# Optimization experiments

Hardware: AMD Instinct MI355X
Metric: run time of the kernel (lower is better)

## Reference

```python
import jax, jax.numpy as jnp
import numpy as np

H = 64  # hidden_dim


def _gru_cell(x, h, W_ih, W_hh, b_ih, b_hh):
    # PyTorch GRU gate order: reset (r), update (z), new (n)
    gx = x @ W_ih.T + b_ih            # [B, 3H]
    gh = h @ W_hh.T + b_hh            # [B, 3H]
    xr, xz, xn = jnp.split(gx, 3, axis=-1)
    hr, hz, hn = jnp.split(gh, 3, axis=-1)
    r = jax.nn.sigmoid(xr + hr)
    z = jax.nn.sigmoid(xz + hz)
    n = jnp.tanh(xn + r * hn)
    return (1.0 - z) * n + z * h


def setup_inputs() -> dict:
    key = jax.random.key(0)
    ks = jax.random.split(key, 11)
    B, T, F_in, A = 1024, 512, 128, 18
    s = 0.05
    return {
        "state": jax.random.normal(ks[0], (B, T, F_in), dtype=jnp.float32),
        "W_ih_l0": jax.random.normal(ks[1], (3 * H, F_in), dtype=jnp.float32) * s,
        "W_hh_l0": jax.random.normal(ks[2], (3 * H, H), dtype=jnp.float32) * s,
        "b_ih_l0": jax.random.normal(ks[3], (3 * H,), dtype=jnp.float32) * s,
        "b_hh_l0": jax.random.normal(ks[4], (3 * H,), dtype=jnp.float32) * s,
        "W_ih_l1": jax.random.normal(ks[5], (3 * H, H), dtype=jnp.float32) * s,
        "W_hh_l1": jax.random.normal(ks[6], (3 * H, H), dtype=jnp.float32) * s,
        "b_ih_l1": jax.random.normal(ks[7], (3 * H,), dtype=jnp.float32) * s,
        "b_hh_l1": jax.random.normal(ks[8], (3 * H,), dtype=jnp.float32) * s,
        "fc3_w": jax.random.normal(ks[9], (A, H), dtype=jnp.float32) * s,
        "fc3_b": jax.random.normal(ks[10], (A,), dtype=jnp.float32) * s,
    }


def reference(state, W_ih_l0, W_hh_l0, b_ih_l0, b_hh_l0,
              W_ih_l1, W_hh_l1, b_ih_l1, b_hh_l1, fc3_w, fc3_b):
    B = state.shape[0]
    h0 = jnp.zeros((B, H), dtype=state.dtype)
    h1 = jnp.zeros((B, H), dtype=state.dtype)
    xs = jnp.swapaxes(state, 0, 1)  # [T, B, F]

    def step(carry, x_t):
        h0, h1 = carry
        h0 = _gru_cell(x_t, h0, W_ih_l0, W_hh_l0, b_ih_l0, b_hh_l0)
        h1 = _gru_cell(h0, h1, W_ih_l1, W_hh_l1, b_ih_l1, b_hh_l1)
        return (h0, h1), None

    (_, h1_last), _ = jax.lax.scan(step, (h0, h1), xs)
    # out[:, -1] of the top GRU layer == final h1; then relu -> linear
    actions = jax.nn.relu(h1_last) @ fc3_w.T + fc3_b
    return actions
```

## Files before the change

### kernel.cpp

```cpp
#include <hip/hip_runtime.h>


#define Tn 512
#define Fn 128
#define Hn 64
#define An 18
#define HS 72

typedef _Float16 half8 __attribute__((ext_vector_type(8)));
typedef float f32x4 __attribute__((ext_vector_type(4)));

#define MFMA(a, b, c) __builtin_amdgcn_mfma_f32_16x16x32_f16((a), (b), (c), 0, 0, 0)

static __device__ __forceinline__ float sigm(float x) {
    return __builtin_amdgcn_rcpf(1.0f + __builtin_amdgcn_exp2f(-1.4426950408889634f * x));
}
static __device__ __forceinline__ float tanh_f(float x) {
    return 2.0f * __builtin_amdgcn_rcpf(1.0f + __builtin_amdgcn_exp2f(-2.8853900817779268f * x)) - 1.0f;
}

__global__ __launch_bounds__(768) void gru_fused(
    const float* __restrict__ state,
    const float* __restrict__ Wih0, const float* __restrict__ Whh0,
    const float* __restrict__ bih0, const float* __restrict__ bhh0,
    const float* __restrict__ Wih1, const float* __restrict__ Whh1,
    const float* __restrict__ bih1, const float* __restrict__ bhh1,
    const float* __restrict__ fcw, const float* __restrict__ fcb,
    float* __restrict__ out)
{
    const int tid  = threadIdx.x;
    const int wv12 = tid >> 6;
    const int lane = tid & 63, c = lane & 15, q = lane >> 4;
    const int wv   = wv12 & 3;
    const int r0   = blockIdx.x * 16;
    const int gc   = wv * 16 + c;
    const int role = (wv12 < 4) ? 0 : (wv12 < 8 ? 1 : 2);

    __shared__ __align__(16) float    gxring[2][4][3][64][4];
    __shared__ __align__(16) _Float16 h0buf[2][16 * HS];
    __shared__ __align__(16) _Float16 h1buf[2][16 * HS];
    __shared__ float fbuf[16 * 64];

    for (int i = tid; i < 2 * 16 * HS; i += 768) {
        (&h0buf[0][0])[i] = (_Float16)0.0f;
        (&h1buf[0][0])[i] = (_Float16)0.0f;
    }

    half8 W[12];
    f32x4 bias0, bias1, bias2, bias3;
    f32x4 xf32[8];
    f32x4 hreg = {0.f, 0.f, 0.f, 0.f};
    const float* srow = state + (size_t)(r0 + c) * (Tn * Fn);

    if (role == 0) {
#pragma unroll
        for (int gsel = 0; gsel < 3; ++gsel) {
            const int g = gsel * 64 + gc;
#pragma unroll
            for (int ks = 0; ks < 4; ++ks) {
                const float* p = Wih0 + g * Fn + ks * 32 + q * 8;
#pragma unroll
                for (int j = 0; j < 8; ++j) W[gsel * 4 + ks][j] = (_Float16)p[j];
            }
        }
        {
            const float b0 = bih0[gc] + bhh0[gc];
            const float b1 = bih0[64 + gc] + bhh0[64 + gc];
            const float b2 = bih0[128 + gc];
            bias0 = (f32x4){b0, b0, b0, b0};
            bias1 = (f32x4){b1, b1, b1, b1};
            bias2 = (f32x4){b2, b2, b2, b2};
        }
#pragma unroll
        for (int ks = 0; ks < 4; ++ks) {
            xf32[2 * ks]     = *(const f32x4*)(srow + ks * 32 + q * 8);
            xf32[2 * ks + 1] = *(const f32x4*)(srow + ks * 32 + q * 8 + 4);
        }
        half8 xf[4];
#pragma unroll
        for (int ks = 0; ks < 4; ++ks)
#pragma unroll
            for (int i = 0; i < 4; ++i) {
                xf[ks][i]     = (_Float16)xf32[2 * ks][i];
                xf[ks][4 + i] = (_Float16)xf32[2 * ks + 1][i];
            }
        f32x4 a0 = bias0, a1 = bias1, a2 = bias2;
#pragma unroll
        for (int ks = 0; ks < 4; ++ks) {
            a0 = MFMA(xf[ks], W[ks], a0);
            a1 = MFMA(xf[ks], W[4 + ks], a1);
            a2 = MFMA(xf[ks], W[8 + ks], a2);
        }
        *(f32x4*)&gxring[0][wv][0][lane][0] = a0;
        *(f32x4*)&gxring[0][wv][1][lane][0] = a1;
        *(f32x4*)&gxring[0][wv][2][lane][0] = a2;
#pragma unroll
        for (int ks = 0; ks < 4; ++ks) {
            xf32[2 * ks]     = *(const f32x4*)(srow + Fn + ks * 32 + q * 8);
            xf32[2 * ks + 1] = *(const f32x4*)(srow + Fn + ks * 32 + q * 8 + 4);
        }
    } else if (role == 1) {
#pragma unroll
        for (int gsel = 0; gsel < 3; ++gsel) {
            const int g = gsel * 64 + gc;
#pragma unroll
            for (int ks = 0; ks < 2; ++ks) {
                const float* p = Whh0 + g * Hn + ks * 32 + q * 8;
#pragma unroll
                for (int j = 0; j < 8; ++j) W[gsel * 2 + ks][j] = (_Float16)p[j];
            }
        }
        const float bhn = bhh0[128 + gc];
        bias3 = (f32x4){bhn, bhn, bhn, bhn};
    } else {
#pragma unroll
        for (int gsel = 0; gsel < 3; ++gsel) {
            const int g = gsel * 64 + gc;
#pragma unroll
            for (int ks = 0; ks < 2; ++ks) {
                const float* pa = Wih1 + g * Hn + ks * 32 + q * 8;
                const float* pb = Whh1 + g * Hn + ks * 32 + q * 8;
#pragma unroll
                for (int j = 0; j < 8; ++j) {
                    W[gsel * 2 + ks][j]     = (_Float16)pa[j];
                    W[6 + gsel * 2 + ks][j] = (_Float16)pb[j];
                }
            }
        }
        const float br = bih1[gc] + bhh1[gc];
        const float bz = bih1[64 + gc] + bhh1[64 + gc];
        const float bxn = bih1[128 + gc];
        const float bhn = bhh1[128 + gc];
        bias0 = (f32x4){br, br, br, br};
        bias1 = (f32x4){bz, bz, bz, bz};
        bias2 = (f32x4){bxn, bxn, bxn, bxn};
        bias3 = (f32x4){bhn, bhn, bhn, bhn};
    }

    const int ardr = c * HS + q * 8;
    const int wrow = (q * 4) * HS + gc;

    for (int t = 0; t <= Tn; ++t) {
        __syncthreads();
        const int pr = (t & 1) ^ 1, pw = t & 1;
        if (role == 0) {
            if (t < Tn - 1) {
                half8 xf[4];
#pragma unroll
                for (int ks = 0; ks < 4; ++ks)
#pragma unroll
                    for (int i = 0; i < 4; ++i) {
                        xf[ks][i]     = (_Float16)xf32[2 * ks][i];
                        xf[ks][4 + i] = (_Float16)xf32[2 * ks + 1][i];
                    }
                const int tnx = (t + 2 < Tn) ? (t + 2) : (Tn - 1);
#pragma unroll
                for (int ks = 0; ks < 4; ++ks) {
                    xf32[2 * ks]     = *(const f32x4*)(srow + (size_t)tnx * Fn + ks * 32 + q * 8);
                    xf32[2 * ks + 1] = *(const f32x4*)(srow + (size_t)tnx * Fn + ks * 32 + q * 8 + 4);
                }
                f32x4 a0 = bias0, a1 = bias1, a2 = bias2;
#pragma unroll
                for (int ks = 0; ks < 4; ++ks) {
                    a0 = MFMA(xf[ks], W[ks], a0);
                    a1 = MFMA(xf[ks], W[4 + ks], a1);
                    a2 = MFMA(xf[ks], W[8 + ks], a2);
                }
                const int slot = (t + 1) & 1;
                *(f32x4*)&gxring[slot][wv][0][lane][0] = a0;
                *(f32x4*)&gxring[slot][wv][1][lane][0] = a1;
                *(f32x4*)&gxring[slot][wv][2][lane][0] = a2;
            }
        } else if (role == 1) {
            if (t < Tn) {
                f32x4 accr  = *(const f32x4*)&gxring[t & 1][wv][0][lane][0];
                f32x4 accz  = *(const f32x4*)&gxring[t & 1][wv][1][lane][0];
                f32x4 accxn = *(const f32x4*)&gxring[t & 1][wv][2][lane][0];
                const half8 hf0 = *(const half8*)&h0buf[pr][ardr];
                const half8 hf1 = *(const half8*)&h0buf[pr][ardr + 32];
                accr = MFMA(hf0, W[0], accr);
                accr = MFMA(hf1, W[1], accr);
                accz = MFMA(hf0, W[2], accz);
                accz = MFMA(hf1, W[3], accz);
                f32x4 acchn = MFMA(hf0, W[4], bias3);
                acchn = MFMA(hf1, W[5], acchn);
#pragma unroll
                for (int i = 0; i < 4; ++i) {
                    const float rg = sigm(accr[i]);
                    const float zg = sigm(accz[i]);
                    const float ng = tanh_f(accxn[i] + rg * acchn[i]);
                    hreg[i] = ng + zg * (hreg[i] - ng);
                }
#pragma unroll
                for (int i = 0; i < 4; ++i) h0buf[pw][wrow + i * HS] = (_Float16)hreg[i];
            }
        } else {
            if (t >= 1) {
                const half8 xf0 = *(const half8*)&h0buf[pr][ardr];
                const half8 xf1 = *(const half8*)&h0buf[pr][ardr + 32];
                const half8 hf0 = *(const half8*)&h1buf[pw][ardr];
                const half8 hf1 = *(const half8*)&h1buf[pw][ardr + 32];
                f32x4 accr = MFMA(xf0, W[0], bias0);
                accr = MFMA(xf1, W[1], accr);
                f32x4 accz = MFMA(xf0, W[2], bias1);
                accz = MFMA(xf1, W[3], accz);
                f32x4 accxn = MFMA(xf0, W[4], bias2);
                accxn = MFMA(xf1, W[5], accxn);
                accr = MFMA(hf0, W[6], accr);
                accr = MFMA(hf1, W[7], accr);
                accz = MFMA(hf0, W[8], accz);
                accz = MFMA(hf1, W[9], accz);
                f32x4 acchn = MFMA(hf0, W[10], bias3);
                acchn = MFMA(hf1, W[11], acchn);
#pragma unroll
                for (int i = 0; i < 4; ++i) {
                    const float rg = sigm(accr[i]);
                    const float zg = sigm(accz[i]);
                    const float ng = tanh_f(accxn[i] + rg * acchn[i]);
                    hreg[i] = ng + zg * (hreg[i] - ng);
                }
#pragma unroll
                for (int i = 0; i < 4; ++i) h1buf[pr][wrow + i * HS] = (_Float16)hreg[i];
            }
        }
    }

    if (role == 2) {
#pragma unroll
        for (int i = 0; i < 4; ++i) fbuf[(q * 4 + i) * 64 + gc] = fmaxf(hreg[i], 0.0f);
    }
    __syncthreads();
    for (int idx = tid; idx < 16 * An; idx += 768) {
        const int row = idx / An, a = idx - row * An;
        float acc = fcb[a];
#pragma unroll 16
        for (int k = 0; k < Hn; ++k) acc += fbuf[row * 64 + k] * fcw[a * Hn + k];
        out[(size_t)(r0 + row) * An + a] = acc;
    }
}

extern "C" void kernel_launch(void* const* d_in, const int* in_sizes, int n_in,
                              void* d_out, int out_size, void* d_ws, size_t ws_size,
                              hipStream_t stream) {
    const float* state = (const float*)d_in[0];
    const float* Wih0  = (const float*)d_in[1];
    const float* Whh0  = (const float*)d_in[2];
    const float* bih0  = (const float*)d_in[3];
    const float* bhh0  = (const float*)d_in[4];
    const float* Wih1  = (const float*)d_in[5];
    const float* Whh1  = (const float*)d_in[6];
    const float* bih1  = (const float*)d_in[7];
    const float* bhh1  = (const float*)d_in[8];
    const float* fcw   = (const float*)d_in[9];
    const float* fcb   = (const float*)d_in[10];
    float* out = (float*)d_out;

    gru_fused<<<64, 768, 0, stream>>>(state, Wih0, Whh0, bih0, bhh0,
                                      Wih1, Whh1, bih1, bhh1, fcw, fcb, out);
}
```

Measured before the change: 740.4 us.

## Merge layer-0 input projection into recurrent waves, drop LDS gx ring

Removes the separate role of four waves that computed the layer-0 input projection and passed it through an LDS ring buffer. Layer-0 waves now compute the x-projection themselves each step, from x converted a step ahead, alongside the h-projection. The block shrinks from 12 to 8 waves, and MFMA chains are split into independent partial accumulators that are summed afterwards. s_setprio is raised around the MFMA sections. This cuts LDS traffic and barrier participants but lengthens the per-step critical path of the layer-0 waves and raises their register pressure.

Result: slower. 800.7 us (+8.1%).

```diff
diff --git a/kernel.cpp b/kernel.cpp
--- a/kernel.cpp
+++ b/kernel.cpp
@@ -19,7 +19,7 @@
     return 2.0f * __builtin_amdgcn_rcpf(1.0f + __builtin_amdgcn_exp2f(-2.8853900817779268f * x)) - 1.0f;
 }
 
-__global__ __launch_bounds__(768) void gru_fused(
+__global__ __launch_bounds__(512) void gru_fused(
     const float* __restrict__ state,
     const float* __restrict__ Wih0, const float* __restrict__ Whh0,
     const float* __restrict__ bih0, const float* __restrict__ bhh0,
@@ -29,30 +29,30 @@
     float* __restrict__ out)
 {
     const int tid  = threadIdx.x;
-    const int wv12 = tid >> 6;
+    const int wv8  = tid >> 6;
     const int lane = tid & 63, c = lane & 15, q = lane >> 4;
-    const int wv   = wv12 & 3;
+    const int wv   = wv8 & 3;
     const int r0   = blockIdx.x * 16;
     const int gc   = wv * 16 + c;
-    const int role = (wv12 < 4) ? 0 : (wv12 < 8 ? 1 : 2);
-
-    __shared__ __align__(16) float    gxring[2][4][3][64][4];
+    const int roleB = (wv8 >= 4);
+
     __shared__ __align__(16) _Float16 h0buf[2][16 * HS];
     __shared__ __align__(16) _Float16 h1buf[2][16 * HS];
     __shared__ float fbuf[16 * 64];
 
-    for (int i = tid; i < 2 * 16 * HS; i += 768) {
+    for (int i = tid; i < 2 * 16 * HS; i += 512) {
         (&h0buf[0][0])[i] = (_Float16)0.0f;
         (&h1buf[0][0])[i] = (_Float16)0.0f;
     }
 
-    half8 W[12];
+    half8 W[18];
     f32x4 bias0, bias1, bias2, bias3;
     f32x4 xf32[8];
+    half8 xf[4];
     f32x4 hreg = {0.f, 0.f, 0.f, 0.f};
     const float* srow = state + (size_t)(r0 + c) * (Tn * Fn);
 
-    if (role == 0) {
+    if (!roleB) {
 #pragma unroll
         for (int gsel = 0; gsel < 3; ++gsel) {
             const int g = gsel * 64 + gc;
@@ -61,22 +61,29 @@
                 const float* p = Wih0 + g * Fn + ks * 32 + q * 8;
 #pragma unroll
                 for (int j = 0; j < 8; ++j) W[gsel * 4 + ks][j] = (_Float16)p[j];
+            }
+#pragma unroll
+            for (int ks = 0; ks < 2; ++ks) {
+                const float* p = Whh0 + g * Hn + ks * 32 + q * 8;
+#pragma unroll
+                for (int j = 0; j < 8; ++j) W[12 + gsel * 2 + ks][j] = (_Float16)p[j];
             }
         }
         {
             const float b0 = bih0[gc] + bhh0[gc];
             const float b1 = bih0[64 + gc] + bhh0[64 + gc];
             const float b2 = bih0[128 + gc];
+            const float b3 = bhh0[128 + gc];
             bias0 = (f32x4){b0, b0, b0, b0};
             bias1 = (f32x4){b1, b1, b1, b1};
             bias2 = (f32x4){b2, b2, b2, b2};
+            bias3 = (f32x4){b3, b3, b3, b3};
         }
 #pragma unroll
         for (int ks = 0; ks < 4; ++ks) {
             xf32[2 * ks]     = *(const f32x4*)(srow + ks * 32 + q * 8);
             xf32[2 * ks + 1] = *(const f32x4*)(srow + ks * 32 + q * 8 + 4);
         }
-        half8 xf[4];
 #pragma unroll
         for (int ks = 0; ks < 4; ++ks)
 #pragma unroll
@@ -84,34 +91,11 @@
                 xf[ks][i]     = (_Float16)xf32[2 * ks][i];
                 xf[ks][4 + i] = (_Float16)xf32[2 * ks + 1][i];
             }
-        f32x4 a0 = bias0, a1 = bias1, a2 = bias2;
-#pragma unroll
-        for (int ks = 0; ks < 4; ++ks) {
-            a0 = MFMA(xf[ks], W[ks], a0);
-            a1 = MFMA(xf[ks], W[4 + ks], a1);
-            a2 = MFMA(xf[ks], W[8 + ks], a2);
-        }
-        *(f32x4*)&gxring[0][wv][0][lane][0] = a0;
-        *(f32x4*)&gxring[0][wv][1][lane][0] = a1;
-        *(f32x4*)&gxring[0][wv][2][lane][0] = a2;
 #pragma unroll
         for (int ks = 0; ks < 4; ++ks) {
             xf32[2 * ks]     = *(const f32x4*)(srow + Fn + ks * 32 + q * 8);
             xf32[2 * ks + 1] = *(const f32x4*)(srow + Fn + ks * 32 + q * 8 + 4);
         }
-    } else if (role == 1) {
-#pragma unroll
-        for (int gsel = 0; gsel < 3; ++gsel) {
-            const int g = gsel * 64 + gc;
-#pragma unroll
-            for (int ks = 0; ks < 2; ++ks) {
-                const float* p = Whh0 + g * Hn + ks * 32 + q * 8;
-#pragma unroll
-                for (int j = 0; j < 8; ++j) W[gsel * 2 + ks][j] = (_Float16)p[j];
-            }
-        }
-        const float bhn = bhh0[128 + gc];
-        bias3 = (f32x4){bhn, bhn, bhn, bhn};
     } else {
 #pragma unroll
         for (int gsel = 0; gsel < 3; ++gsel) {
@@ -127,68 +111,61 @@
                 }
             }
         }
-        const float br = bih1[gc] + bhh1[gc];
-        const float bz = bih1[64 + gc] + bhh1[64 + gc];
+        const float br_ = bih1[gc] + bhh1[gc];
+        const float bz_ = bih1[64 + gc] + bhh1[64 + gc];
         const float bxn = bih1[128 + gc];
         const float bhn = bhh1[128 + gc];
-        bias0 = (f32x4){br, br, br, br};
-        bias1 = (f32x4){bz, bz, bz, bz};
+        bias0 = (f32x4){br_, br_, br_, br_};
+        bias1 = (f32x4){bz_, bz_, bz_, bz_};
         bias2 = (f32x4){bxn, bxn, bxn, bxn};
         bias3 = (f32x4){bhn, bhn, bhn, bhn};
     }
 
     const int ardr = c * HS + q * 8;
     const int wrow = (q * 4) * HS + gc;
+    const f32x4 z4 = {0.f, 0.f, 0.f, 0.f};
 
     for (int t = 0; t <= Tn; ++t) {
         __syncthreads();
         const int pr = (t & 1) ^ 1, pw = t & 1;
-        if (role == 0) {
-            if (t < Tn - 1) {
-                half8 xf[4];
-#pragma unroll
-                for (int ks = 0; ks < 4; ++ks)
-#pragma unroll
-                    for (int i = 0; i < 4; ++i) {
-                        xf[ks][i]     = (_Float16)xf32[2 * ks][i];
-                        xf[ks][4 + i] = (_Float16)xf32[2 * ks + 1][i];
-                    }
-                const int tnx = (t + 2 < Tn) ? (t + 2) : (Tn - 1);
-#pragma unroll
-                for (int ks = 0; ks < 4; ++ks) {
-                    xf32[2 * ks]     = *(const f32x4*)(srow + (size_t)tnx * Fn + ks * 32 + q * 8);
-                    xf32[2 * ks + 1] = *(const f32x4*)(srow + (size_t)tnx * Fn + ks * 32 + q * 8 + 4);
-                }
-                f32x4 a0 = bias0, a1 = bias1, a2 = bias2;
-#pragma unroll
-                for (int ks = 0; ks < 4; ++ks) {
-                    a0 = MFMA(xf[ks], W[ks], a0);
-                    a1 = MFMA(xf[ks], W[4 + ks], a1);
-                    a2 = MFMA(xf[ks], W[8 + ks], a2);
-                }
-                const int slot = (t + 1) & 1;
-                *(f32x4*)&gxring[slot][wv][0][lane][0] = a0;
-                *(f32x4*)&gxring[slot][wv][1][lane][0] = a1;
-                *(f32x4*)&gxring[slot][wv][2][lane][0] = a2;
-            }
-        } else if (role == 1) {
+        if (!roleB) {
             if (t < Tn) {
-                f32x4 accr  = *(const f32x4*)&gxring[t & 1][wv][0][lane][0];
-                f32x4 accz  = *(const f32x4*)&gxring[t & 1][wv][1][lane][0];
-                f32x4 accxn = *(const f32x4*)&gxring[t & 1][wv][2][lane][0];
                 const half8 hf0 = *(const half8*)&h0buf[pr][ardr];
                 const half8 hf1 = *(const half8*)&h0buf[pr][ardr + 32];
-                accr = MFMA(hf0, W[0], accr);
-                accr = MFMA(hf1, W[1], accr);
-                accz = MFMA(hf0, W[2], accz);
-                accz = MFMA(hf1, W[3], accz);
-                f32x4 acchn = MFMA(hf0, W[4], bias3);
-                acchn = MFMA(hf1, W[5], acchn);
+                __builtin_amdgcn_s_setprio(1);
+                f32x4 ar = MFMA(xf[0], W[0], bias0);  ar = MFMA(xf[1], W[1], ar);
+                f32x4 az = MFMA(xf[0], W[4], bias1);  az = MFMA(xf[1], W[5], az);
+                f32x4 an = MFMA(xf[0], W[8], bias2);  an = MFMA(xf[1], W[9], an);
+                f32x4 br = MFMA(xf[2], W[2], z4);     br = MFMA(xf[3], W[3], br);
+                f32x4 bz = MFMA(xf[2], W[6], z4);     bz = MFMA(xf[3], W[7], bz);
+                f32x4 bn = MFMA(xf[2], W[10], z4);    bn = MFMA(xf[3], W[11], bn);
+                br = MFMA(hf0, W[12], br);  br = MFMA(hf1, W[13], br);
+                bz = MFMA(hf0, W[14], bz);  bz = MFMA(hf1, W[15], bz);
+                f32x4 hn = MFMA(hf0, W[16], bias3);  hn = MFMA(hf1, W[17], hn);
+                __builtin_amdgcn_s_setprio(0);
+                if (t < Tn - 1) {
+#pragma unroll
+                    for (int ks = 0; ks < 4; ++ks)
+#pragma unroll
+                        for (int i = 0; i < 4; ++i) {
+                            xf[ks][i]     = (_Float16)xf32[2 * ks][i];
+                            xf[ks][4 + i] = (_Float16)xf32[2 * ks + 1][i];
+                        }
+                    const int tnx = (t + 2 < Tn) ? (t + 2) : (Tn - 1);
+#pragma unroll
+                    for (int ks = 0; ks < 4; ++ks) {
+                        xf32[2 * ks]     = *(const f32x4*)(srow + (size_t)tnx * Fn + ks * 32 + q * 8);
+                        xf32[2 * ks + 1] = *(const f32x4*)(srow + (size_t)tnx * Fn + ks * 32 + q * 8 + 4);
+                    }
+                }
+                const f32x4 accr  = ar + br;
+                const f32x4 accz  = az + bz;
+                const f32x4 accxn = an + bn;
 #pragma unroll
                 for (int i = 0; i < 4; ++i) {
                     const float rg = sigm(accr[i]);
                     const float zg = sigm(accz[i]);
-                    const float ng = tanh_f(accxn[i] + rg * acchn[i]);
+                    const float ng = tanh_f(accxn[i] + rg * hn[i]);
                     hreg[i] = ng + zg * (hreg[i] - ng);
                 }
 #pragma unroll
@@ -200,23 +177,21 @@
                 const half8 xf1 = *(const half8*)&h0buf[pr][ardr + 32];
                 const half8 hf0 = *(const half8*)&h1buf[pw][ardr];
                 const half8 hf1 = *(const half8*)&h1buf[pw][ardr + 32];
-                f32x4 accr = MFMA(xf0, W[0], bias0);
-                accr = MFMA(xf1, W[1], accr);
-                f32x4 accz = MFMA(xf0, W[2], bias1);
-                accz = MFMA(xf1, W[3], accz);
-                f32x4 accxn = MFMA(xf0, W[4], bias2);
-                accxn = MFMA(xf1, W[5], accxn);
-                accr = MFMA(hf0, W[6], accr);
-                accr = MFMA(hf1, W[7], accr);
-                accz = MFMA(hf0, W[8], accz);
-                accz = MFMA(hf1, W[9], accz);
-                f32x4 acchn = MFMA(hf0, W[10], bias3);
-                acchn = MFMA(hf1, W[11], acchn);
+                __builtin_amdgcn_s_setprio(1);
+                f32x4 xr = MFMA(xf0, W[0], bias0);  xr = MFMA(xf1, W[1], xr);
+                f32x4 xz = MFMA(xf0, W[2], bias1);  xz = MFMA(xf1, W[3], xz);
+                f32x4 xn = MFMA(xf0, W[4], bias2);  xn = MFMA(xf1, W[5], xn);
+                f32x4 hr = MFMA(hf0, W[6], z4);     hr = MFMA(hf1, W[7], hr);
+                f32x4 hz = MFMA(hf0, W[8], z4);     hz = MFMA(hf1, W[9], hz);
+                f32x4 hn = MFMA(hf0, W[10], bias3); hn = MFMA(hf1, W[11], hn);
+                __builtin_amdgcn_s_setprio(0);
+                const f32x4 accr = xr + hr;
+                const f32x4 accz = xz + hz;
 #pragma unroll
                 for (int i = 0; i < 4; ++i) {
                     const float rg = sigm(accr[i]);
                     const float zg = sigm(accz[i]);
-                    const float ng = tanh_f(accxn[i] + rg * acchn[i]);
+                    const float ng = tanh_f(xn[i] + rg * hn[i]);
                     hreg[i] = ng + zg * (hreg[i] - ng);
                 }
 #pragma unroll
@@ -225,12 +200,12 @@
         }
     }
 
-    if (role == 2) {
+    if (roleB) {
 #pragma unroll
         for (int i = 0; i < 4; ++i) fbuf[(q * 4 + i) * 64 + gc] = fmaxf(hreg[i], 0.0f);
     }
     __syncthreads();
-    for (int idx = tid; idx < 16 * An; idx += 768) {
+    for (int idx = tid; idx < 16 * An; idx += 512) {
         const int row = idx / An, a = idx - row * An;
         float acc = fcb[a];
 #pragma unroll 16
@@ -255,6 +230,6 @@
     const float* fcb   = (const float*)d_in[10];
     float* out = (float*)d_out;
 
-    gru_fused<<<64, 768, 0, stream>>>(state, Wih0, Whh0, bih0, bhh0,
+    gru_fused<<<64, 512, 0, stream>>>(state, Wih0, Whh0, bih0, bhh0,
                                       Wih1, Whh1, bih1, bhh1, fcw, fcb, out);
 }
```
